# Kernel optimization log

Measured on AMD Instinct MI355X. Metric: run time of the kernel, lower is better.

Reference implementation:

```python
import jax, jax.numpy as jnp
import numpy as np

H = 768        # hidden_size == embedding_dim (forced by GRU input 3*H)
S = 512        # seq_len
V = 30522      # vocab_size
MAXLEN = 32    # decode steps
B = 8
NEG = -1e6


def setup_inputs() -> dict:
    key = jax.random.key(0)
    ks = jax.random.split(key, 12)
    sd = 0.02
    return {
        "encoder_outputs": jax.random.normal(ks[0], (B, S, H), jnp.float32),
        "inputs": jax.random.randint(ks[1], (B, S), 0, V),
        "cls_to": 101,
        "sep_to": 102,
        "emb": jax.random.normal(ks[2], (V, H), jnp.float32) * sd,
        "attn_w": jax.random.normal(ks[3], (H, H), jnp.float32) * sd,
        "attn_b": jnp.zeros((H,), jnp.float32),
        "copy_w": jax.random.normal(ks[4], (H, H), jnp.float32) * sd,
        "copy_b": jnp.zeros((H,), jnp.float32),
        "gru_w_ih": jax.random.normal(ks[5], (3 * H, 3 * H), jnp.float32) * sd,
        "gru_w_hh": jax.random.normal(ks[6], (3 * H, H), jnp.float32) * sd,
        "gru_b_ih": jnp.zeros((3 * H,), jnp.float32),
        "gru_b_hh": jnp.zeros((3 * H,), jnp.float32),
        "out_w": jax.random.normal(ks[7], (V, H), jnp.float32) * sd,
        "out_b": jnp.zeros((V,), jnp.float32),
    }


def _gru_cell(x, h, w_ih, w_hh, b_ih, b_hh):
    # PyTorch GRU cell, gate order (r, z, n)
    gi = x @ w_ih.T + b_ih          # [B, 3H]
    gh = h @ w_hh.T + b_hh          # [B, 3H]
    gi_r, gi_z, gi_n = jnp.split(gi, 3, axis=-1)
    gh_r, gh_z, gh_n = jnp.split(gh, 3, axis=-1)
    r = jax.nn.sigmoid(gi_r + gh_r)
    z = jax.nn.sigmoid(gi_z + gh_z)
    n = jnp.tanh(gi_n + r * gh_n)
    return (1.0 - z) * n + z * h


def reference(encoder_outputs, inputs, cls_to, sep_to, emb, attn_w, attn_b,
              copy_w, copy_b, gru_w_ih, gru_w_hh, gru_b_ih, gru_b_hh,
              out_w, out_b):
    dtype = encoder_outputs.dtype
    ext = V + S  # extended vocab (vocab + seq positions)
    one_hot = jax.nn.one_hot(inputs, ext, dtype=dtype)          # [B, S, V+S]
    missing = (one_hot.sum(axis=1) == 0).at[:, 0].set(True)     # [B, V+S]

    def step(carry, _):
        hidden, idx, sel = carry  # [B,H], [B] int, [B,H]
        # attention
        th = hidden @ attn_w.T + attn_b                          # [B,H]
        attn_scores = jnp.einsum('bsh,bh->bs', encoder_outputs, th)
        attn_weights = jax.nn.softmax(attn_scores, axis=-1)
        context = jnp.einsum('bs,bsh->bh', attn_weights, encoder_outputs)
        # embed previous token (OOV -> UNK id 3; note original uses strict >)
        idx_c = jnp.where(idx > V, 3, idx)
        embedded = emb[idx_c]                                    # [B,H]
        # GRU step
        x = jnp.concatenate([context, sel, embedded], axis=-1)   # [B,3H]
        h = _gru_cell(x, hidden, gru_w_ih, gru_w_hh, gru_b_ih, gru_b_hh)
        # copy scores
        th2 = h @ copy_w.T + copy_b
        copy_score_seq = jnp.einsum('bsh,bh->bs', encoder_outputs, th2)  # [B,S]
        copy_scores = jnp.einsum('bs,bsv->bv', copy_score_seq, one_hot)  # [B,V+S]
        copy_scores = jnp.where(missing, NEG, copy_scores)
        # generation scores
        gen = (h @ out_w.T + out_b).at[:, 0].set(NEG)            # [B,V]
        combined = jnp.concatenate([gen, copy_scores], axis=-1)  # [B,2V+S]
        probs = jax.nn.softmax(combined, axis=-1)
        gen_probs = jnp.concatenate(
            [probs[:, :V], jnp.zeros((B, S), dtype)], axis=-1)   # [B,V+S]
        final_probs = gen_probs + probs[:, V:]
        log_probs = jnp.log(final_probs + 1e-10)                 # [B,V+S]
        sampled = jnp.argmax(log_probs, axis=-1)                 # [B]
        # selective read for next step
        pos = jnp.take_along_axis(one_hot, sampled[:, None, None], axis=2)[..., 0]  # [B,S]
        sel_scores = pos * copy_score_seq
        denom = jnp.maximum(jnp.sum(jnp.abs(sel_scores), axis=1, keepdims=True), 1e-12)
        sel_new = jnp.einsum('bs,bsh->bh', sel_scores / denom, encoder_outputs)
        return (h, sampled, sel_new), (log_probs, sampled)

    init = (jnp.zeros((B, H), dtype),
            jnp.ones((B,), jnp.int32),
            jnp.zeros((B, H), dtype))
    _, (logps, samples) = jax.lax.scan(step, init, None, length=MAXLEN - 1)

    sos = jnp.zeros((B, ext), dtype).at[:, 0].set(cls_to)
    decoder_outputs = jnp.concatenate(
        [sos[:, None, :], jnp.swapaxes(logps, 0, 1)], axis=1)    # [B,MAXLEN,V+S]
    sampled_idxs = jnp.concatenate(
        [jnp.ones((B, 1), samples.dtype), samples.T], axis=1)    # [B,MAXLEN]
    return decoder_outputs, sampled_idxs
```

## Files before the change

kernel.cpp:

```cpp
#include <hip/hip_runtime.h>
#include <hip/hip_bf16.h>
#include <math.h>

#define HDIM 768
#define SDIM 512
#define VDIM 30522
#define BDIM 8
#define TLEN 32
#define H3   2304
#define VT   31034
#define NEGV -1.0e6f
#define OFF2 ((size_t)BDIM * TLEN * VT)
#define NSUB 32
#define SSL  16
#define VSL  954
#define VSLICE 3816
#define NROWS (HDIM + VDIM + HDIM + H3)

__global__ __launch_bounds__(256) void boot_kernel(
    float* __restrict__ dout, const int* __restrict__ cls,
    float* __restrict__ hA, float* __restrict__ x,
    const float* __restrict__ emb, float* __restrict__ thb,
    float* __restrict__ ghb, const float* __restrict__ attn_b,
    const float* __restrict__ b_hh)
{
    int gidx = blockIdx.x * 256 + threadIdx.x;
    int stride = gridDim.x * 256;
    float clsv = (float)cls[0];
    for (int i = gidx; i < BDIM * VT; i += stride) {
        int b = i / VT, v = i % VT;
        dout[(size_t)b * TLEN * VT + v] = (v == 0) ? clsv : 0.f;
    }
    if (gidx < BDIM) dout[OFF2 + (size_t)gidx * TLEN] = 1.0f;
    for (int i = gidx; i < BDIM * HDIM; i += stride) {
        int b = i / HDIM, j = i % HDIM;
        hA[i] = 0.f;
        x[b * H3 + HDIM + j] = 0.f;
        x[b * H3 + 2 * HDIM + j] = emb[HDIM + j];
        thb[i] = attn_b[j];
    }
    for (int i = gidx; i < BDIM * H3; i += stride)
        ghb[i] = b_hh[i % H3];
}

__global__ __launch_bounds__(64) void grufull_kernel(
    const float* __restrict__ w_ih, const float* __restrict__ b_ih,
    const float* __restrict__ x, const float* __restrict__ ghb,
    const float* __restrict__ hin, float* __restrict__ hout)
{
    int lane = threadIdx.x;
    int j = blockIdx.x;

    const float4* wr = (const float4*)(w_ih + (size_t)j * H3);
    const float4* wz = (const float4*)(w_ih + (size_t)(HDIM + j) * H3);
    const float4* wn = (const float4*)(w_ih + (size_t)(2 * HDIM + j) * H3);

    float ar[8], az[8], an[8];
#pragma unroll
    for (int b = 0; b < 8; b++) { ar[b] = 0.f; az[b] = 0.f; an[b] = 0.f; }

    for (int k4 = lane; k4 < H3 / 4; k4 += 64) {
        float4 w4r = wr[k4], w4z = wz[k4], w4n = wn[k4];
#pragma unroll
        for (int b = 0; b < 8; b++) {
            float4 x4 = ((const float4*)(x + b * H3))[k4];
            ar[b] += w4r.x * x4.x + w4r.y * x4.y + w4r.z * x4.z + w4r.w * x4.w;
            az[b] += w4z.x * x4.x + w4z.y * x4.y + w4z.z * x4.z + w4z.w * x4.w;
            an[b] += w4n.x * x4.x + w4n.y * x4.y + w4n.z * x4.z + w4n.w * x4.w;
        }
    }
#pragma unroll
    for (int b = 0; b < 8; b++) {
        float vr = ar[b], vz = az[b], vn = an[b];
        for (int off = 32; off; off >>= 1) {
            vr += __shfl_down(vr, off, 64);
            vz += __shfl_down(vz, off, 64);
            vn += __shfl_down(vn, off, 64);
        }
        ar[b] = vr; az[b] = vz; an[b] = vn;
    }
    if (lane == 0) {
        float bi_r = b_ih[j], bi_z = b_ih[HDIM + j], bi_n = b_ih[2 * HDIM + j];
#pragma unroll
        for (int b = 0; b < 8; b++) {
            float gir = ar[b] + bi_r;
            float giz = az[b] + bi_z;
            float gin = an[b] + bi_n;
            float ghr = ghb[b * H3 + j];
            float ghz = ghb[b * H3 + HDIM + j];
            float ghn = ghb[b * H3 + 2 * HDIM + j];
            float r = 1.f / (1.f + expf(-(gir + ghr)));
            float z = 1.f / (1.f + expf(-(giz + ghz)));
            float n = tanhf(gin + r * ghn);
            hout[b * HDIM + j] = (1.f - z) * n + z * hin[b * HDIM + j];
        }
    }
}

struct RowT { const float* w; const float* bias; float* dst; int stride; int neg; };

__device__ __forceinline__ RowT row_info(
    int r,
    const float* copy_w, const float* copy_b,
    const float* out_w,  const float* out_b,
    const float* attn_w, const float* attn_b,
    const float* w_hh,   const float* b_hh,
    float* th2, float* gen, float* thb, float* ghb)
{
    RowT t;
    if (r < HDIM) {
        t.w = copy_w + (size_t)r * HDIM; t.bias = copy_b + r;
        t.dst = th2 + r; t.stride = HDIM; t.neg = 0;
    } else if (r < HDIM + VDIM) {
        int v = r - HDIM;
        t.w = out_w + (size_t)v * HDIM; t.bias = out_b + v;
        t.dst = gen + v; t.stride = VDIM; t.neg = (v == 0);
    } else if (r < 2 * HDIM + VDIM) {
        int rr = r - HDIM - VDIM;
        t.w = attn_w + (size_t)rr * HDIM; t.bias = attn_b + rr;
        t.dst = thb + rr; t.stride = HDIM; t.neg = 0;
    } else {
        int rr = r - 2 * HDIM - VDIM;
        t.w = w_hh + (size_t)rr * HDIM; t.bias = b_hh + rr;
        t.dst = ghb + rr; t.stride = H3; t.neg = 0;
    }
    return t;
}

__global__ __launch_bounds__(256) void bigmv_kernel(
    const float* __restrict__ copy_w, const float* __restrict__ copy_b,
    const float* __restrict__ out_w,  const float* __restrict__ out_b,
    const float* __restrict__ attn_w, const float* __restrict__ attn_b,
    const float* __restrict__ w_hh,   const float* __restrict__ b_hh,
    const float* __restrict__ hp, float* __restrict__ th2,
    float* __restrict__ gen, float* __restrict__ thb,
    float* __restrict__ ghb)
{
    int wid = threadIdx.x >> 6, lane = threadIdx.x & 63;
    int r0 = blockIdx.x * 16 + wid * 4;
    if (r0 >= NROWS) return;

    int rc1 = min(r0 + 1, NROWS - 1);
    int rc2 = min(r0 + 2, NROWS - 1), rc3 = min(r0 + 3, NROWS - 1);
    RowT t0 = row_info(r0,  copy_w, copy_b, out_w, out_b, attn_w, attn_b,
                       w_hh, b_hh, th2, gen, thb, ghb);
    RowT t1 = row_info(rc1, copy_w, copy_b, out_w, out_b, attn_w, attn_b,
                       w_hh, b_hh, th2, gen, thb, ghb);
    RowT t2 = row_info(rc2, copy_w, copy_b, out_w, out_b, attn_w, attn_b,
                       w_hh, b_hh, th2, gen, thb, ghb);
    RowT t3 = row_info(rc3, copy_w, copy_b, out_w, out_b, attn_w, attn_b,
                       w_hh, b_hh, th2, gen, thb, ghb);

    float a0[8], a1[8], a2[8], a3[8];
#pragma unroll
    for (int b = 0; b < 8; b++) { a0[b] = 0.f; a1[b] = 0.f; a2[b] = 0.f; a3[b] = 0.f; }

    const float4* w0 = (const float4*)t0.w;
    const float4* w1 = (const float4*)t1.w;
    const float4* w2 = (const float4*)t2.w;
    const float4* w3 = (const float4*)t3.w;
    const float4* xb = (const float4*)hp;

#pragma unroll
    for (int i = 0; i < 3; i++) {
        int k4 = lane + i * 64;
        float4 q0 = w0[k4], q1 = w1[k4], q2 = w2[k4], q3 = w3[k4];
#pragma unroll
        for (int b = 0; b < 8; b++) {
            float4 x4 = xb[b * 192 + k4];
            a0[b] += q0.x * x4.x + q0.y * x4.y + q0.z * x4.z + q0.w * x4.w;
            a1[b] += q1.x * x4.x + q1.y * x4.y + q1.z * x4.z + q1.w * x4.w;
            a2[b] += q2.x * x4.x + q2.y * x4.y + q2.z * x4.z + q2.w * x4.w;
            a3[b] += q3.x * x4.x + q3.y * x4.y + q3.z * x4.z + q3.w * x4.w;
        }
    }
#pragma unroll
    for (int b = 0; b < 8; b++) {
        float v0 = a0[b], v1 = a1[b], v2 = a2[b], v3 = a3[b];
        for (int off = 32; off; off >>= 1) {
            v0 += __shfl_down(v0, off, 64);
            v1 += __shfl_down(v1, off, 64);
            v2 += __shfl_down(v2, off, 64);
            v3 += __shfl_down(v3, off, 64);
        }
        a0[b] = v0; a1[b] = v1; a2[b] = v2; a3[b] = v3;
    }
    if (lane == 0) {
        float bb0 = t0.bias[0], bb1 = t1.bias[0], bb2 = t2.bias[0], bb3 = t3.bias[0];
#pragma unroll
        for (int b = 0; b < 8; b++) {
            t0.dst[(size_t)b * t0.stride] = t0.neg ? NEGV : a0[b] + bb0;
            if (r0 + 1 < NROWS) t1.dst[(size_t)b * t1.stride] = t1.neg ? NEGV : a1[b] + bb1;
            if (r0 + 2 < NROWS) t2.dst[(size_t)b * t2.stride] = t2.neg ? NEGV : a2[b] + bb2;
            if (r0 + 3 < NROWS) t3.dst[(size_t)b * t3.stride] = t3.neg ? NEGV : a3[b] + bb3;
        }
    }
}

__global__ __launch_bounds__(512) void combo_kernel(
    const float* __restrict__ enc, const float* __restrict__ thb,
    const float* __restrict__ th2, float* __restrict__ css,
    float* __restrict__ atC, float* __restrict__ atM, float* __restrict__ atZ,
    const float* __restrict__ gen, float* __restrict__ gM,
    float* __restrict__ gZ, int do_cg)
{
    __shared__ float sth[HDIM];
    __shared__ float sth2[HDIM];
    __shared__ float swe[SSL];
    __shared__ float red[8];
    int blk = blockIdx.x, b = blk >> 5, sub = blk & 31;
    int tid = threadIdx.x, wid = tid >> 6, lane = tid & 63;
    int slo = sub * SSL;

    for (int i = tid; i < HDIM; i += 512) {
        sth[i]  = thb[b * HDIM + i];
        sth2[i] = th2[b * HDIM + i];
    }
    __syncthreads();

    for (int j = 0; j < 2; j++) {
        int sl = wid * 2 + j, s = slo + sl;
        const float4* er = (const float4*)(enc + ((size_t)b * SDIM + s) * HDIM);
        float a1 = 0.f, a2 = 0.f;
#pragma unroll
        for (int i = 0; i < 3; i++) {
            float4 e = er[lane + i * 64];
            float4 t1 = ((const float4*)sth)[lane + i * 64];
            float4 t2 = ((const float4*)sth2)[lane + i * 64];
            a1 += e.x * t1.x + e.y * t1.y + e.z * t1.z + e.w * t1.w;
            a2 += e.x * t2.x + e.y * t2.y + e.z * t2.z + e.w * t2.w;
        }
        for (int off = 32; off; off >>= 1) {
            a1 += __shfl_down(a1, off, 64);
            a2 += __shfl_down(a2, off, 64);
        }
        if (lane == 0) {
            swe[sl] = a1;
            if (do_cg) css[b * SDIM + s] = a2;
        }
    }
    __syncthreads();

    if (tid == 0) {
        float m = swe[0];
        for (int i = 1; i < SSL; i++) m = fmaxf(m, swe[i]);
        float z = 0.f;
        for (int i = 0; i < SSL; i++) { float e = expf(swe[i] - m); swe[i] = e; z += e; }
        atM[b * NSUB + sub] = m;
        atZ[b * NSUB + sub] = z;
    }
    __syncthreads();

    for (int col = tid; col < HDIM; col += 512) {
        float acc = 0.f;
        const float* eb = enc + ((size_t)b * SDIM + slo) * HDIM + col;
#pragma unroll
        for (int s2 = 0; s2 < SSL; s2++) acc += swe[s2] * eb[s2 * HDIM];
        atC[((size_t)b * NSUB + sub) * HDIM + col] = acc;
    }

    if (!do_cg) return;

    int vlo = sub * VSL, vhi = min(VDIM, vlo + VSL);
    const float* grow = gen + (size_t)b * VDIM;
    float m = -INFINITY;
    for (int v = vlo + tid; v < vhi; v += 512) m = fmaxf(m, grow[v]);
    for (int off = 32; off; off >>= 1) m = fmaxf(m, __shfl_xor(m, off, 64));
    if (lane == 0) red[wid] = m;
    __syncthreads();
    float M = red[0];
#pragma unroll
    for (int w = 1; w < 8; w++) M = fmaxf(M, red[w]);
    float z = 0.f;
    for (int v = vlo + tid; v < vhi; v += 512) z += expf(grow[v] - M);
    for (int off = 32; off; off >>= 1) z += __shfl_xor(z, off, 64);
    __syncthreads();
    if (lane == 0) red[wid] = z;
    __syncthreads();
    if (tid == 0) {
        float Z = 0.f;
#pragma unroll
        for (int w = 0; w < 8; w++) Z += red[w];
        gM[b * NSUB + sub] = M;
        gZ[b * NSUB + sub] = Z;
    }
}

__global__ __launch_bounds__(1024) void tailc_kernel(
    const float* __restrict__ gen, const float* __restrict__ css,
    const int* __restrict__ inputs, const float* __restrict__ genM,
    const float* __restrict__ genZ, float* __restrict__ dout,
    float* __restrict__ argV, int* __restrict__ argI, int t)
{
    __shared__ int   toks[SDIM];
    __shared__ float csss[SDIM];
    __shared__ float aggv[SDIM];
    __shared__ unsigned char ffl[SDIM];
    __shared__ float redf[1024];
    __shared__ int   redi[1024];
    int blk = blockIdx.x, b = blk >> 3, sub = blk & 7;
    int tid = threadIdx.x;

    if (tid < SDIM) {
        toks[tid] = inputs[b * SDIM + tid];
        csss[tid] = css[b * SDIM + tid];
    }
    __syncthreads();

    if (tid < SDIM) {
        int tok = toks[tid]; int isf = 0; float agg = -INFINITY;
        if (tok != 0) {
            isf = 1;
            for (int s2 = 0; s2 < tid; s2++)
                if (toks[s2] == tok) { isf = 0; break; }
            if (isf) {
                float ss = 0.f;
                for (int s2 = tid; s2 < SDIM; s2++)
                    if (toks[s2] == tok) ss += csss[s2];
                agg = ss;
            }
        }
        ffl[tid] = (unsigned char)isf;
        aggv[tid] = agg;
    }
    __syncthreads();

    redf[tid] = (tid < SDIM && ffl[tid]) ? aggv[tid] : -INFINITY;
    __syncthreads();
    for (int off = 512; off; off >>= 1) {
        if (tid < off) redf[tid] = fmaxf(redf[tid], redf[tid + off]);
        __syncthreads();
    }
    float m9 = redf[0]; __syncthreads();
    redf[tid] = (tid < SDIM && ffl[tid] && m9 > -INFINITY)
                    ? expf(aggv[tid] - m9) : 0.f;
    __syncthreads();
    for (int off = 512; off; off >>= 1) {
        if (tid < off) redf[tid] += redf[tid + off];
        __syncthreads();
    }
    float z9 = redf[0]; __syncthreads();

    float M = genM[b * NSUB + 0];
#pragma unroll
    for (int i = 1; i < NSUB; i++) M = fmaxf(M, genM[b * NSUB + i]);
    if (m9 > -INFINITY) M = fmaxf(M, m9);
    float Z = 0.f;
#pragma unroll
    for (int i = 0; i < NSUB; i++)
        Z += genZ[b * NSUB + i] * expf(genM[b * NSUB + i] - M);
    if (m9 > -INFINITY) Z += z9 * expf(m9 - M);
    float invZ = 1.f / Z;

    const float* grow = gen + (size_t)b * VDIM;
    float* orow = dout + ((size_t)b * TLEN + t + 1) * VT;
    int vlo = sub * VSLICE, vhi = min(VDIM, vlo + VSLICE);
    float best = -INFINITY; int bidx = 2147483647;
    for (int v = vlo + tid; v < vhi; v += 1024) {
        float pg = expf(grow[v] - M) * invZ;
        float lp = logf(pg + 1e-10f);
        orow[v] = lp;
        if (lp > best) { best = lp; bidx = v; }
    }
    if (sub == 0 && tid < SDIM) orow[VDIM + tid] = logf(1e-10f);
    __syncthreads();

    if (tid < SDIM && ffl[tid]) {
        int tok = toks[tid];
        if (tok >= vlo && tok < vhi) {
            float pc = expf(aggv[tid] - M) * invZ;
            float pg = expf(grow[tok] - M) * invZ;
            float lp = logf(pg + pc + 1e-10f);
            orow[tok] = lp;
            if (lp > best || (lp == best && tok < bidx)) { best = lp; bidx = tok; }
        }
    }
    redf[tid] = best; redi[tid] = bidx; __syncthreads();
    for (int off = 512; off; off >>= 1) {
        if (tid < off) {
            float v2 = redf[tid + off]; int i2 = redi[tid + off];
            if (v2 > redf[tid] || (v2 == redf[tid] && i2 < redi[tid])) {
                redf[tid] = v2; redi[tid] = i2;
            }
        }
        __syncthreads();
    }
    if (tid == 0) { argV[b * 8 + sub] = redf[0]; argI[b * 8 + sub] = redi[0]; }
}

__global__ __launch_bounds__(1024) void mix_kernel(
    const float* __restrict__ enc, const float* __restrict__ css,
    const int* __restrict__ inputs, const float* __restrict__ argV,
    const int* __restrict__ argI, const float* __restrict__ emb,
    float* __restrict__ dout, float* __restrict__ x,
    const float* __restrict__ atC, const float* __restrict__ atM,
    const float* __restrict__ atZ, int t, int do_tail)
{
    __shared__ int   toks[SDIM];
    __shared__ float csss[SDIM];
    __shared__ float redf[1024];
    __shared__ int   mlist[SDIM];
    __shared__ float mscore[SDIM];
    __shared__ int   wcnt[16], woff[16];
    __shared__ int   mtot;
    int bid = blockIdx.x, tid = threadIdx.x;

    if (bid >= BDIM) {
        int b = bid - BDIM;
        if (tid < HDIM) {
            float M = atM[b * NSUB];
#pragma unroll
            for (int i = 1; i < NSUB; i++) M = fmaxf(M, atM[b * NSUB + i]);
            float Z = 0.f, acc = 0.f;
#pragma unroll
            for (int i = 0; i < NSUB; i++) {
                float sc = expf(atM[b * NSUB + i] - M);
                Z += atZ[b * NSUB + i] * sc;
                acc += atC[((size_t)b * NSUB + i) * HDIM + tid] * sc;
            }
            x[b * H3 + tid] = acc / Z;
        }
        return;
    }
    if (!do_tail) return;

    int b = bid;
    float best = argV[b * 8 + 0]; int samp = argI[b * 8 + 0];
#pragma unroll
    for (int i = 1; i < 8; i++) {
        float v = argV[b * 8 + i];
        if (v > best) { best = v; samp = argI[b * 8 + i]; }
    }
    if (tid == 0) dout[OFF2 + (size_t)b * TLEN + t + 1] = (float)samp;

    if (tid < SDIM) {
        toks[tid] = inputs[b * SDIM + tid];
        csss[tid] = css[b * SDIM + tid];
    }
    __syncthreads();

    int flag = (tid < SDIM) ? (toks[tid] == samp) : 0;
    redf[tid] = flag ? fabsf(csss[tid]) : 0.f;
    __syncthreads();
    for (int off = 512; off; off >>= 1) {
        if (tid < off) redf[tid] += redf[tid + off];
        __syncthreads();
    }
    float den = fmaxf(redf[0], 1e-12f);
    __syncthreads();

    unsigned long long mk = __ballot(flag);
    int wv = tid >> 6, ln = tid & 63;
    if (ln == 0) wcnt[wv] = __popcll(mk);
    __syncthreads();
    if (tid == 0) {
        int o = 0;
        for (int w = 0; w < 16; w++) { woff[w] = o; o += wcnt[w]; }
        mtot = o;
    }
    __syncthreads();
    if (flag) {
        int pos = woff[wv] + __popcll(mk & ((1ULL << ln) - 1ULL));
        mlist[pos] = tid;
        mscore[pos] = csss[tid] / den;
    }
    __syncthreads();
    int mc = mtot;

    if (tid < HDIM) {
        float sel = 0.f;
        for (int mI = 0; mI < mc; mI++)
            sel += mscore[mI] * enc[((size_t)b * SDIM + mlist[mI]) * HDIM + tid];
        x[b * H3 + HDIM + tid] = sel;
        int ic = (samp > VDIM) ? 3 : samp;
        if (ic >= VDIM) ic = VDIM - 1;
        x[b * H3 + 2 * HDIM + tid] = emb[(size_t)ic * HDIM + tid];
    }
}

extern "C" void kernel_launch(void* const* d_in, const int* in_sizes, int n_in,
                              void* d_out, int out_size, void* d_ws, size_t ws_size,
                              hipStream_t stream)
{
    const float* enc    = (const float*)d_in[0];
    const int*   inputs = (const int*)d_in[1];
    const int*   cls    = (const int*)d_in[2];
    const float* emb    = (const float*)d_in[4];
    const float* attn_w = (const float*)d_in[5];
    const float* attn_b = (const float*)d_in[6];
    const float* copy_w = (const float*)d_in[7];
    const float* copy_b = (const float*)d_in[8];
    const float* w_ih   = (const float*)d_in[9];
    const float* w_hh   = (const float*)d_in[10];
    const float* b_ih   = (const float*)d_in[11];
    const float* b_hh   = (const float*)d_in[12];
    const float* out_w  = (const float*)d_in[13];
    const float* out_b  = (const float*)d_in[14];
    float* dout = (float*)d_out;

    float* ws   = (float*)d_ws;
    float* hA   = ws;
    float* hB   = hA  + BDIM * HDIM;
    float* x    = hB  + BDIM * HDIM;
    float* thb  = x   + BDIM * H3;
    float* ghb  = thb + BDIM * HDIM;
    float* th2  = ghb + BDIM * H3;
    float* gen  = th2 + BDIM * HDIM;
    float* css  = gen + (size_t)BDIM * VDIM;
    float* atC  = css + BDIM * SDIM;
    float* atM  = atC + (size_t)BDIM * NSUB * HDIM;
    float* atZ  = atM + BDIM * NSUB;
    float* gM   = atZ + BDIM * NSUB;
    float* gZ   = gM  + BDIM * NSUB;
    float* argV = gZ  + BDIM * NSUB;
    int*   argI = (int*)(argV + 64);

    boot_kernel<<<512, 256, 0, stream>>>(dout, cls, hA, x, emb, thb, ghb,
                                         attn_b, b_hh);
    combo_kernel<<<256, 512, 0, stream>>>(enc, thb, th2, css, atC, atM, atZ,
                                          gen, gM, gZ, 0);
    mix_kernel<<<16, 1024, 0, stream>>>(enc, css, inputs, argV, argI, emb,
                                        dout, x, atC, atM, atZ, 0, 0);

    for (int t = 0; t < TLEN - 1; t++) {
        const float* hin  = (t & 1) ? hB : hA;
        float*       hout = (t & 1) ? hA : hB;
        grufull_kernel<<<HDIM, 64, 0, stream>>>(w_ih, b_ih, x, ghb, hin, hout);
        bigmv_kernel<<<(NROWS + 15) / 16, 256, 0, stream>>>(
            copy_w, copy_b, out_w, out_b, attn_w, attn_b, w_hh, b_hh,
            hout, th2, gen, thb, ghb);
        combo_kernel<<<256, 512, 0, stream>>>(enc, thb, th2, css, atC, atM, atZ,
                                              gen, gM, gZ, 1);
        tailc_kernel<<<64, 1024, 0, stream>>>(gen, css, inputs, gM, gZ,
                                              dout, argV, argI, t);
        mix_kernel<<<16, 1024, 0, stream>>>(enc, css, inputs, argV, argI, emb,
                                            dout, x, atC, atM, atZ, t, 1);
    }
}
```

Measured before the change: 3.298 ms.

## Widen GRU, tail and combo kernels for more parallelism and register reuse

The GRU input projection now uses four waves per output row, each covering a quarter of the K dimension, with partial sums combined through shared memory. The tail kernel splits the vocabulary into 32 slices per batch row instead of 8, launching 256 blocks, and the argmax merge reads 32 partials. The combo kernel keeps encoder rows in registers from the score pass and reuses them for the weighted context sum through a shared-memory reduction, instead of reloading encoder data from global memory. Adding an occupancy hint to bigmv may constrain register allocation.

```diff
diff --git a/kernel.cpp b/kernel.cpp
--- a/kernel.cpp
+++ b/kernel.cpp
@@ -14,7 +14,6 @@
 #define NSUB 32
 #define SSL  16
 #define VSL  954
-#define VSLICE 3816
 #define NROWS (HDIM + VDIM + HDIM + H3)
 
 __global__ __launch_bounds__(256) void boot_kernel(
@@ -43,12 +42,13 @@
         ghb[i] = b_hh[i % H3];
 }
 
-__global__ __launch_bounds__(64) void grufull_kernel(
+__global__ __launch_bounds__(256) void grufull_kernel(
     const float* __restrict__ w_ih, const float* __restrict__ b_ih,
     const float* __restrict__ x, const float* __restrict__ ghb,
     const float* __restrict__ hin, float* __restrict__ hout)
 {
-    int lane = threadIdx.x;
+    __shared__ float gp[4][3][BDIM];
+    int tid = threadIdx.x, w = tid >> 6, lane = tid & 63;
     int j = blockIdx.x;
 
     const float4* wr = (const float4*)(w_ih + (size_t)j * H3);
@@ -59,7 +59,8 @@
 #pragma unroll
     for (int b = 0; b < 8; b++) { ar[b] = 0.f; az[b] = 0.f; an[b] = 0.f; }
 
-    for (int k4 = lane; k4 < H3 / 4; k4 += 64) {
+    int k0 = w * 144;
+    for (int k4 = k0 + lane; k4 < k0 + 144; k4 += 64) {
         float4 w4r = wr[k4], w4z = wz[k4], w4n = wn[k4];
 #pragma unroll
         for (int b = 0; b < 8; b++) {
@@ -80,20 +81,26 @@
         ar[b] = vr; az[b] = vz; an[b] = vn;
     }
     if (lane == 0) {
-        float bi_r = b_ih[j], bi_z = b_ih[HDIM + j], bi_n = b_ih[2 * HDIM + j];
 #pragma unroll
         for (int b = 0; b < 8; b++) {
-            float gir = ar[b] + bi_r;
-            float giz = az[b] + bi_z;
-            float gin = an[b] + bi_n;
-            float ghr = ghb[b * H3 + j];
-            float ghz = ghb[b * H3 + HDIM + j];
-            float ghn = ghb[b * H3 + 2 * HDIM + j];
-            float r = 1.f / (1.f + expf(-(gir + ghr)));
-            float z = 1.f / (1.f + expf(-(giz + ghz)));
-            float n = tanhf(gin + r * ghn);
-            hout[b * HDIM + j] = (1.f - z) * n + z * hin[b * HDIM + j];
-        }
+            gp[w][0][b] = ar[b];
+            gp[w][1][b] = az[b];
+            gp[w][2][b] = an[b];
+        }
+    }
+    __syncthreads();
+    if (tid < BDIM) {
+        int b = tid;
+        float gir = gp[0][0][b] + gp[1][0][b] + gp[2][0][b] + gp[3][0][b] + b_ih[j];
+        float giz = gp[0][1][b] + gp[1][1][b] + gp[2][1][b] + gp[3][1][b] + b_ih[HDIM + j];
+        float gin = gp[0][2][b] + gp[1][2][b] + gp[2][2][b] + gp[3][2][b] + b_ih[2 * HDIM + j];
+        float ghr = ghb[b * H3 + j];
+        float ghz = ghb[b * H3 + HDIM + j];
+        float ghn = ghb[b * H3 + 2 * HDIM + j];
+        float r = 1.f / (1.f + expf(-(gir + ghr)));
+        float z = 1.f / (1.f + expf(-(giz + ghz)));
+        float n = tanhf(gin + r * ghn);
+        hout[b * HDIM + j] = (1.f - z) * n + z * hin[b * HDIM + j];
     }
 }
 
@@ -127,7 +134,7 @@
     return t;
 }
 
-__global__ __launch_bounds__(256) void bigmv_kernel(
+__global__ __launch_bounds__(256, 8) void bigmv_kernel(
     const float* __restrict__ copy_w, const float* __restrict__ copy_b,
     const float* __restrict__ out_w,  const float* __restrict__ out_b,
     const float* __restrict__ attn_w, const float* __restrict__ attn_b,
@@ -208,6 +215,7 @@
     __shared__ float sth2[HDIM];
     __shared__ float swe[SSL];
     __shared__ float red[8];
+    __shared__ float4 part[8][HDIM / 4];
     int blk = blockIdx.x, b = blk >> 5, sub = blk & 31;
     int tid = threadIdx.x, wid = tid >> 6, lane = tid & 63;
     int slo = sub * SSL;
@@ -218,6 +226,8 @@
     }
     __syncthreads();
 
+    float4 e0[3], e1[3];
+#pragma unroll
     for (int j = 0; j < 2; j++) {
         int sl = wid * 2 + j, s = slo + sl;
         const float4* er = (const float4*)(enc + ((size_t)b * SDIM + s) * HDIM);
@@ -225,6 +235,7 @@
 #pragma unroll
         for (int i = 0; i < 3; i++) {
             float4 e = er[lane + i * 64];
+            if (j == 0) e0[i] = e; else e1[i] = e;
             float4 t1 = ((const float4*)sth)[lane + i * 64];
             float4 t2 = ((const float4*)sth2)[lane + i * 64];
             a1 += e.x * t1.x + e.y * t1.y + e.z * t1.z + e.w * t1.w;
@@ -251,12 +262,27 @@
     }
     __syncthreads();
 
-    for (int col = tid; col < HDIM; col += 512) {
-        float acc = 0.f;
-        const float* eb = enc + ((size_t)b * SDIM + slo) * HDIM + col;
-#pragma unroll
-        for (int s2 = 0; s2 < SSL; s2++) acc += swe[s2] * eb[s2 * HDIM];
-        atC[((size_t)b * NSUB + sub) * HDIM + col] = acc;
+    {
+        float wq0 = swe[wid * 2], wq1 = swe[wid * 2 + 1];
+#pragma unroll
+        for (int i = 0; i < 3; i++) {
+            float4 p;
+            p.x = wq0 * e0[i].x + wq1 * e1[i].x;
+            p.y = wq0 * e0[i].y + wq1 * e1[i].y;
+            p.z = wq0 * e0[i].z + wq1 * e1[i].z;
+            p.w = wq0 * e0[i].w + wq1 * e1[i].w;
+            part[wid][lane + i * 64] = p;
+        }
+    }
+    __syncthreads();
+    if (tid < HDIM / 4) {
+        float4 acc = part[0][tid];
+#pragma unroll
+        for (int w = 1; w < 8; w++) {
+            float4 p = part[w][tid];
+            acc.x += p.x; acc.y += p.y; acc.z += p.z; acc.w += p.w;
+        }
+        ((float4*)(atC + ((size_t)b * NSUB + sub) * HDIM))[tid] = acc;
     }
 
     if (!do_cg) return;
@@ -298,7 +324,7 @@
     __shared__ unsigned char ffl[SDIM];
     __shared__ float redf[1024];
     __shared__ int   redi[1024];
-    int blk = blockIdx.x, b = blk >> 3, sub = blk & 7;
+    int blk = blockIdx.x, b = blk >> 5, sub = blk & 31;
     int tid = threadIdx.x;
 
     if (tid < SDIM) {
@@ -354,7 +380,7 @@
 
     const float* grow = gen + (size_t)b * VDIM;
     float* orow = dout + ((size_t)b * TLEN + t + 1) * VT;
-    int vlo = sub * VSLICE, vhi = min(VDIM, vlo + VSLICE);
+    int vlo = sub * VSL, vhi = min(VDIM, vlo + VSL);
     float best = -INFINITY; int bidx = 2147483647;
     for (int v = vlo + tid; v < vhi; v += 1024) {
         float pg = expf(grow[v] - M) * invZ;
@@ -385,7 +411,7 @@
         }
         __syncthreads();
     }
-    if (tid == 0) { argV[b * 8 + sub] = redf[0]; argI[b * 8 + sub] = redi[0]; }
+    if (tid == 0) { argV[b * NSUB + sub] = redf[0]; argI[b * NSUB + sub] = redi[0]; }
 }
 
 __global__ __launch_bounds__(1024) void mix_kernel(
@@ -425,11 +451,11 @@
     if (!do_tail) return;
 
     int b = bid;
-    float best = argV[b * 8 + 0]; int samp = argI[b * 8 + 0];
-#pragma unroll
-    for (int i = 1; i < 8; i++) {
-        float v = argV[b * 8 + i];
-        if (v > best) { best = v; samp = argI[b * 8 + i]; }
+    float best = argV[b * NSUB + 0]; int samp = argI[b * NSUB + 0];
+#pragma unroll
+    for (int i = 1; i < NSUB; i++) {
+        float v = argV[b * NSUB + i];
+        if (v > best) { best = v; samp = argI[b * NSUB + i]; }
     }
     if (tid == 0) dout[OFF2 + (size_t)b * TLEN + t + 1] = (float)samp;
 
@@ -513,7 +539,7 @@
     float* gM   = atZ + BDIM * NSUB;
     float* gZ   = gM  + BDIM * NSUB;
     float* argV = gZ  + BDIM * NSUB;
-    int*   argI = (int*)(argV + 64);
+    int*   argI = (int*)(argV + BDIM * NSUB);
 
     boot_kernel<<<512, 256, 0, stream>>>(dout, cls, hA, x, emb, thb, ghb,
                                          attn_b, b_hh);
@@ -525,14 +551,14 @@
     for (int t = 0; t < TLEN - 1; t++) {
         const float* hin  = (t & 1) ? hB : hA;
         float*       hout = (t & 1) ? hA : hB;
-        grufull_kernel<<<HDIM, 64, 0, stream>>>(w_ih, b_ih, x, ghb, hin, hout);
+        grufull_kernel<<<HDIM, 256, 0, stream>>>(w_ih, b_ih, x, ghb, hin, hout);
         bigmv_kernel<<<(NROWS + 15) / 16, 256, 0, stream>>>(
             copy_w, copy_b, out_w, out_b, attn_w, attn_b, w_hh, b_hh,
             hout, th2, gen, thb, ghb);
         combo_kernel<<<256, 512, 0, stream>>>(enc, thb, th2, css, atC, atM, atZ,
                                               gen, gM, gZ, 1);
-        tailc_kernel<<<64, 1024, 0, stream>>>(gen, css, inputs, gM, gZ,
-                                              dout, argV, argI, t);
+        tailc_kernel<<<256, 1024, 0, stream>>>(gen, css, inputs, gM, gZ,
+                                               dout, argV, argI, t);
         mix_kernel<<<16, 1024, 0, stream>>>(enc, css, inputs, argV, argI, emb,
                                             dout, x, atC, atM, atZ, t, 1);
     }
```

After: 4.390 ms. 33.1% more time.
